# Kernel tuning notes

Hardware: AMD Instinct MI355X
Metric: run time of the kernel (lower is better)

The kernel has to match this reference:

```python
import jax, jax.numpy as jnp
import numpy as np

N_QUBITS = 10
N_LAYERS = 2
OUT_FEATURES = 64
N_BATCH = 128


def _apply_ry(state, theta, q, n):
    # state: [B, 2^n] real (RY gates are real), theta: [B]
    B = state.shape[0]
    left = 2 ** q
    right = 2 ** (n - q - 1)
    s = state.reshape(B, left, 2, right)
    half = theta * 0.5
    c = jnp.cos(half)[:, None, None]
    sn = jnp.sin(half)[:, None, None]
    s0 = s[:, :, 0, :]
    s1 = s[:, :, 1, :]
    out = jnp.stack([c * s0 - sn * s1, sn * s0 + c * s1], axis=2)
    return out.reshape(B, -1)


def _apply_cnot(state, q, n):
    # control qubit q, target qubit q+1 (adjacent), real statevector
    B = state.shape[0]
    left = 2 ** q
    right = 2 ** (n - q - 2)
    s = state.reshape(B, left, 2, 2, right)
    flipped = jnp.flip(s[:, :, 1, :, :], axis=2)  # swap target amps where control=1
    out = jnp.stack([s[:, :, 0, :, :], flipped], axis=2)
    return out.reshape(B, -1)


def _zdiag(n):
    # diagonal of H = sum_i Z_i in the computational basis: n - 2*popcount(index)
    idx = np.arange(2 ** n)
    pop = np.array([bin(i).count('1') for i in range(2 ** n)], dtype=np.float32)
    return jnp.asarray(n - 2.0 * pop, dtype=jnp.float32)


def setup_inputs() -> dict:
    key = jax.random.key(0)
    kx, kw = jax.random.split(key)
    x = jax.random.normal(kx, (N_BATCH, N_QUBITS), dtype=jnp.float32)
    weight = jax.random.normal(kw, (OUT_FEATURES, N_QUBITS, N_LAYERS), dtype=jnp.float32)
    return {"x": x, "weight": weight}


def reference(x, weight):
    n_batch, n = x.shape
    out_features, _, n_layers = weight.shape
    B = out_features * n_batch
    # x.repeat(out_features, 1): tile batch across output features
    xb = jnp.tile(x, (out_features, 1))  # [B, n]
    # weight expanded over batch: [O, 1, n, L] -> [O, nb, n, L] -> [B, n, L]
    pb = jnp.broadcast_to(weight[:, None, :, :], (out_features, n_batch, n, n_layers))
    pb = pb.reshape(B, n, n_layers)
    # |0...0> statevector, real since the circuit (RY + CNOT) is real
    state = jnp.zeros((B, 2 ** n), dtype=jnp.float32).at[:, 0].set(1.0)
    # data-encoding layer: RY(x_q) on each qubit
    for q in range(n):
        state = _apply_ry(state, xb[:, q], q, n)
    # variational layers: RY(theta_{q,l}) on each qubit + CNOT ladder entangler
    for l in range(n_layers):
        for q in range(n):
            state = _apply_ry(state, pb[:, q, l], q, n)
        for q in range(n - 1):
            state = _apply_cnot(state, q, n)
    zd = _zdiag(n)
    # energy expectation <psi| sum_i Z_i |psi> (real circuit -> real output)
    out = jnp.einsum('bk,k->b', state * state, zd)  # [B]
    return out.reshape(out_features, n_batch)
```

## Files before the change

### kernel.cpp

```cpp
#include <hip/hip_runtime.h>
#include <math.h>


__global__ void qnn_closed_v13(const float* gx, const float* gw, float* gout) {
    const int circ = (int)blockIdx.x * 64 + (int)threadIdx.x;
    const int f = circ >> 7, b = circ & 127;

    float z[10], xv[10], cc[10], ss[10];
    #pragma unroll
    for (int q = 0; q < 10; ++q) {
        const float th = gx[b * 10 + q] + gw[(f * 10 + q) * 2 + 0];
        z[q]  = cosf(th);
        xv[q] = sinf(th);
        const float ph = gw[(f * 10 + q) * 2 + 1];
        cc[q] = cosf(ph);
        ss[q] = sinf(ph);
    }

    float E = 0.0f;
    #pragma unroll
    for (int k = 0; k < 10; ++k) {
        float v00 = cc[k];
        float v10 = -ss[k] * ((k < 9) ? xv[k + 1] : 1.0f);
        float v01 = 0.0f, v11 = 0.0f;
        #pragma unroll
        for (int j = k - 1; j >= 0; --j) {
            const float zj = z[j + 1], xj = xv[j + 1];
            const float n00 =  cc[j] * (v01 + xj * v10);
            const float n01 =  cc[j] * (zj * v00);
            const float n10 = -ss[j] * (xj * v01 + v10);
            const float n11 = -ss[j] * (zj * v11);
            v00 = n00; v01 = n01; v10 = n10; v11 = n11;
        }
        E += v00 * z[0] + v01 + v10 * xv[0];
    }

    gout[circ] = E;
}

extern "C" void kernel_launch(void* const* d_in, const int* in_sizes, int n_in,
                              void* d_out, int out_size, void* d_ws, size_t ws_size,
                              hipStream_t stream) {
    const float* x = (const float*)d_in[0];
    const float* w = (const float*)d_in[1];
    float* out = (float*)d_out;

    hipLaunchKernelGGL(qnn_closed_v13, dim3(128), dim3(64), 0, stream, x, w, out);
}
```

Measured before the change: 59.00 us.

## Share per-feature weight trig in LDS and use angle-addition for data angles

Launches one block per output feature with one thread per batch element. The first 20 threads compute cos/sin of that feature's weights once and store them in shared memory. Each thread then computes cos/sin of its x angle and combines them with the shared values through angle-addition identities, instead of evaluating 40 transcendentals per thread. The aim is to cut per-thread transcendental work, at the cost of a block barrier and slightly different rounding.

```diff
diff --git a/kernel.cpp b/kernel.cpp
--- a/kernel.cpp
+++ b/kernel.cpp
@@ -2,19 +2,31 @@
 #include <math.h>
 
 
-__global__ void qnn_closed_v13(const float* gx, const float* gw, float* gout) {
-    const int circ = (int)blockIdx.x * 64 + (int)threadIdx.x;
-    const int f = circ >> 7, b = circ & 127;
+__global__ __launch_bounds__(128) void qnn_closed_v14(const float* gx,
+                                                      const float* gw,
+                                                      float* gout) {
+    __shared__ float wc0[10], ws0[10], wc1[10], ws1[10];
+    const int b = (int)threadIdx.x;
+    const int f = (int)blockIdx.x;
+
+    if (b < 20) {
+        const int q = b % 10;
+        const int l = b / 10;
+        const float a = gw[(f * 10 + q) * 2 + l];
+        if (l == 0) { wc0[q] = cosf(a); ws0[q] = sinf(a); }
+        else        { wc1[q] = cosf(a); ws1[q] = sinf(a); }
+    }
+    __syncthreads();
 
     float z[10], xv[10], cc[10], ss[10];
     #pragma unroll
     for (int q = 0; q < 10; ++q) {
-        const float th = gx[b * 10 + q] + gw[(f * 10 + q) * 2 + 0];
-        z[q]  = cosf(th);
-        xv[q] = sinf(th);
-        const float ph = gw[(f * 10 + q) * 2 + 1];
-        cc[q] = cosf(ph);
-        ss[q] = sinf(ph);
+        const float xa = gx[b * 10 + q];
+        const float cx = cosf(xa), sx = sinf(xa);
+        z[q]  = cx * wc0[q] - sx * ws0[q];
+        xv[q] = sx * wc0[q] + cx * ws0[q];
+        cc[q] = wc1[q];
+        ss[q] = ws1[q];
     }
 
     float E = 0.0f;
@@ -35,7 +47,7 @@
         E += v00 * z[0] + v01 + v10 * xv[0];
     }
 
-    gout[circ] = E;
+    gout[f * 128 + b] = E;
 }
 
 extern "C" void kernel_launch(void* const* d_in, const int* in_sizes, int n_in,
@@ -45,5 +57,5 @@
     const float* w = (const float*)d_in[1];
     float* out = (float*)d_out;
 
-    hipLaunchKernelGGL(qnn_closed_v13, dim3(128), dim3(64), 0, stream, x, w, out);
+    hipLaunchKernelGGL(qnn_closed_v14, dim3(64), dim3(128), 0, stream, x, w, out);
 }
```

Result: faster. 56.93 us (-3.5%).
